# Kernel tuning notes

Hardware: AMD Instinct MI355X
Metric: run time of the kernel (lower is better)

Reference implementation:

```python
import jax, jax.numpy as jnp
import numpy as np
import math

D_MODEL = 1024
N_HEADS = 16
HEAD_DIM = D_MODEL // N_HEADS
PAD_INDEX = 0
NEG_INF = -1e9  # matches torch masked_fill value


def setup_inputs() -> dict:
    key = jax.random.key(0)
    ks = jax.random.split(key, 10)
    b, s = 2, 2048
    x = jax.random.normal(ks[0], (b, s, D_MODEL), dtype=jnp.float32)
    input_ids = jax.random.randint(ks[1], (b, s), 0, 32000, dtype=jnp.int64)
    scale = 1.0 / math.sqrt(D_MODEL)
    def lin(k):
        kw, kb = jax.random.split(k)
        W = jax.random.uniform(kw, (D_MODEL, D_MODEL), jnp.float32, -scale, scale)
        bb = jax.random.uniform(kb, (D_MODEL,), jnp.float32, -scale, scale)
        return W, bb
    Wq, bq = lin(ks[2])
    Wk, bk = lin(ks[3])
    Wv, bv = lin(ks[4])
    Wo, bo = lin(ks[5])
    return {"x": x, "input_ids": input_ids,
            "Wq": Wq, "bq": bq, "Wk": Wk, "bk": bk,
            "Wv": Wv, "bv": bv, "Wo": Wo, "bo": bo}


def reference(x, input_ids, Wq, bq, Wk, bk, Wv, bv, Wo, bo):
    b, s, _ = x.shape
    # torch nn.Linear: y = x @ W.T + b
    q = (x @ Wq.T + bq).reshape(b, s, N_HEADS, HEAD_DIM)
    k = (x @ Wk.T + bk).reshape(b, s, N_HEADS, HEAD_DIM)
    v = (x @ Wv.T + bv).reshape(b, s, N_HEADS, HEAD_DIM)
    # scores: [b, h, s, s]
    scores = jnp.einsum('bqhd,bkhd->bhqk', q, k) / math.sqrt(HEAD_DIM)
    pad_mask = (input_ids != PAD_INDEX)[:, None, None, :]          # [b,1,1,s] over keys
    causal = jnp.tril(jnp.ones((s, s), dtype=bool))[None, None]     # [1,1,s,s]
    final_mask = pad_mask & causal
    scores = jnp.where(final_mask, scores, NEG_INF)
    attn = jax.nn.softmax(scores, axis=-1)
    out = jnp.einsum('bhqk,bkhd->bqhd', attn, v).reshape(b, s, D_MODEL)
    return out @ Wo.T + bo
```

## Files before the change

### kernel.cpp

```cpp
#include <hip/hip_runtime.h>

#define DMODEL 1024
#define NHEADS 16
#define HDIM   64
#define BATCH  2
#define SEQ    2048
#define MROWS  (BATCH*SEQ)

typedef __bf16 bf16x8 __attribute__((ext_vector_type(8)));
typedef __bf16 bf16x4 __attribute__((ext_vector_type(4)));
typedef float floatx4 __attribute__((ext_vector_type(4)));

typedef const __attribute__((address_space(1))) void gvoid;
typedef __attribute__((address_space(3))) void lvoid;

template<int V>  struct ICi { static constexpr int  value = V; };
template<bool V> struct ICb { static constexpr bool value = V; };

__global__ void cast_all(const float* __restrict__ x,
                         const float* __restrict__ wq, const float* __restrict__ wk,
                         const float* __restrict__ wv, const float* __restrict__ wo,
                         __bf16* __restrict__ xb, __bf16* __restrict__ wqb,
                         __bf16* __restrict__ wkb, __bf16* __restrict__ wvb,
                         __bf16* __restrict__ wob)
{
  const int i = blockIdx.x * 256 + threadIdx.x;
  const float* s; __bf16* o; int off;
  if (i < MROWS*DMODEL/4) { s = x; o = xb; off = i; }
  else {
    const int r = i - MROWS*DMODEL/4;
    const int w = r >> 18;
    off = r & 262143;
    s = (w == 0) ? wq : (w == 1) ? wk : (w == 2) ? wv : wo;
    o = (w == 0) ? wqb : (w == 1) ? wkb : (w == 2) ? wvb : wob;
  }
  const float4 f = ((const float4*)s)[off];
  bf16x4 v = {(__bf16)f.x, (__bf16)f.y, (__bf16)f.z, (__bf16)f.w};
  *(bf16x4*)(o + off*4) = v;
}

template<int MODE>
__global__ __launch_bounds__(256, 3)
void gemm_nt(const unsigned short* __restrict__ A,
             const unsigned short* __restrict__ W0,
             const unsigned short* __restrict__ W1,
             const unsigned short* __restrict__ W2,
             const float* __restrict__ b0,
             const float* __restrict__ b1,
             const float* __restrict__ b2,
             unsigned short* __restrict__ qout,
             unsigned short* __restrict__ kout,
             unsigned short* __restrict__ vout,
             float* __restrict__ outf)
{
  const int K = DMODEL;
  __shared__ unsigned short As[2][128*32];
  __shared__ unsigned short Bs[2][128*32];
  const int tid  = threadIdx.x;
  const int wid  = tid >> 6;
  const int lane = tid & 63;

  const int lin = blockIdx.x;
  const int wg  = (MODE == 0) ? ((lin & 7)*96 + (lin >> 3))
                              : ((lin & 7)*32 + (lin >> 3));
  const int bx  = (MODE == 0) ? (wg % 24) : (wg & 7);
  const int by  = (MODE == 0) ? (wg / 24) : (wg >> 3);
  const int brow = by * 128;
  const int bcol = bx * 128;
  const int wr = (wid >> 1) * 64;
  const int wc = (wid & 1) * 64;

  int which = 0;
  const unsigned short* Bw = W0;
  const float* bias = b0;
  int bcolL = bcol;
  if (MODE == 0) {
    which = bcol >> 10;
    Bw   = which == 0 ? W0 : which == 1 ? W1 : W2;
    bias = which == 0 ? b0 : which == 1 ? b1 : b2;
    bcolL = bcol & 1023;
  }

  floatx4 acc[4][4] = {};

  const int sr = wid*16 + (lane >> 2);
  const int sc = (lane & 3) * 8;
  const int fr = lane & 15;
  const int fk = (lane >> 4) * 8;

#define GSTAGE(KT, B) do {                                                     \
    _Pragma("unroll")                                                          \
    for (int i_ = 0; i_ < 2; ++i_) {                                           \
      __builtin_amdgcn_global_load_lds(                                        \
          (gvoid*)(A + (size_t)(brow + i_*64 + sr)*K + (KT) + sc),             \
          (lvoid*)(As[B] + i_*2048 + wid*512), 16, 0, 0);                      \
      __builtin_amdgcn_global_load_lds(                                        \
          (gvoid*)(Bw + (size_t)(bcolL + i_*64 + sr)*K + (KT) + sc),           \
          (lvoid*)(Bs[B] + i_*2048 + wid*512), 16, 0, 0);                      \
    }                                                                          \
  } while (0)

  GSTAGE(0, 0);

  for (int kt = 0; kt < K; kt += 32) {
    const int cur = (kt >> 5) & 1;
    if (kt + 32 < K) {
      GSTAGE(kt + 32, cur ^ 1);
      asm volatile("s_waitcnt vmcnt(4)" ::: "memory");
    } else {
      asm volatile("s_waitcnt vmcnt(0)" ::: "memory");
    }
    __builtin_amdgcn_s_barrier();
    __builtin_amdgcn_sched_barrier(0);

    bf16x8 af[4], bfv[4];
#pragma unroll
    for (int m = 0; m < 4; ++m)
      af[m] = *(const bf16x8*)(As[cur] + (wr + m*16 + fr)*32 + fk);
#pragma unroll
    for (int n = 0; n < 4; ++n)
      bfv[n] = *(const bf16x8*)(Bs[cur] + (wc + n*16 + fr)*32 + fk);
    __builtin_amdgcn_s_setprio(1);
#pragma unroll
    for (int m = 0; m < 4; ++m)
#pragma unroll
      for (int n = 0; n < 4; ++n)
        acc[m][n] = __builtin_amdgcn_mfma_f32_16x16x32_bf16(af[m], bfv[n], acc[m][n], 0, 0, 0);
    __builtin_amdgcn_s_setprio(0);
    __builtin_amdgcn_s_barrier();
  }
#undef GSTAGE

  const int er = (lane >> 4) * 4;
  const int ec = lane & 15;
#pragma unroll
  for (int m = 0; m < 4; ++m) {
#pragma unroll
    for (int n = 0; n < 4; ++n) {
      const int colL = bcolL + wc + n*16 + ec;
      const float bv = bias[colL];
      const int rowb = brow + wr + m*16 + er;
      if (MODE == 0) {
        const int bi = rowb >> 11, s = rowb & 2047;
        const int hh = colL >> 6, dd = colL & 63;
        if (which == 2) {
          bf16x4 v4 = {(__bf16)(acc[m][n][0] + bv), (__bf16)(acc[m][n][1] + bv),
                       (__bf16)(acc[m][n][2] + bv), (__bf16)(acc[m][n][3] + bv)};
          *(bf16x4*)((__bf16*)vout + ((size_t)(bi*NHEADS + hh)*HDIM + dd)*SEQ + s) = v4;
        } else {
          __bf16* o = (__bf16*)((which == 0) ? qout : kout);
#pragma unroll
          for (int j = 0; j < 4; ++j)
            o[((size_t)(bi*NHEADS + hh)*SEQ + s + j)*HDIM + dd] = (__bf16)(acc[m][n][j] + bv);
        }
      } else {
#pragma unroll
        for (int j = 0; j < 4; ++j)
          outf[(size_t)(rowb + j)*DMODEL + colL] = acc[m][n][j] + bv;
      }
    }
  }
}

__global__ __launch_bounds__(256, 2)
void attn_fwd(const unsigned short* __restrict__ qb,
              const unsigned short* __restrict__ kb,
              const unsigned short* __restrict__ vtb,
              const int* __restrict__ ids,
              unsigned short* __restrict__ outb)
{
  const int hb = blockIdx.x;
  const int pr = blockIdx.y;
  const int h = hb & 15, bi = hb >> 4;

  const int tid = threadIdx.x, wid = tid >> 6, lane = tid & 63;
  const size_t hoff = (size_t)(bi*NHEADS + h) * SEQ * HDIM;
  const unsigned short* Qh  = qb  + hoff;
  const unsigned short* Kh  = kb  + hoff;
  const unsigned short* Vth = vtb + hoff;

  __shared__ unsigned short Ks[2][128*64];
  __shared__ unsigned short Vs[2][64*128];
  __shared__ unsigned short Ps[4][16*128];

  const int q_   = lane & 15;
  const int hi4  = lane >> 4;
  const int koff = hi4 * 4;
  const float SC2 = 0.125f * 1.44269504088896f;

  const int krow0 = tid >> 3;
  const int ksw   = ((tid & 7) ^ ((tid >> 3) & 7)) * 8;
  const int vrow0 = tid >> 4;
  const int vsw   = ((tid & 15) ^ ((tid >> 4) & 7)) * 8;
  unsigned short* Pw = Ps[wid];

#define STAGE(T, B) do {                                                       \
    const unsigned short* kbase_ = Kh + (size_t)(T)*128*HDIM;                  \
    const unsigned short* vbase_ = Vth + (size_t)(T)*128;                      \
    _Pragma("unroll")                                                          \
    for (int i_ = 0; i_ < 4; ++i_)                                             \
      __builtin_amdgcn_global_load_lds(                                        \
          (gvoid*)(kbase_ + (size_t)(krow0 + i_*32)*HDIM + ksw),               \
          (lvoid*)(Ks[B] + (tid + i_*256)*8), 16, 0, 0);                       \
    _Pragma("unroll")                                                          \
    for (int i_ = 0; i_ < 4; ++i_)                                             \
      __builtin_amdgcn_global_load_lds(                                        \
          (gvoid*)(vbase_ + (size_t)(vrow0 + i_*16)*SEQ + vsw),                \
          (lvoid*)(Vs[B] + (tid + i_*256)*8), 16, 0, 0);                       \
  } while (0)

  for (int half = 0; half < 2; ++half) {
    const int qt = half ? 31 - pr : pr;
    const int qbase = qt * 64;
    const int qg = qbase + wid*16 + q_;
    bf16x8 qf[2];
#pragma unroll
    for (int c = 0; c < 2; ++c)
      qf[c] = *(const bf16x8*)(Qh + (size_t)qg*HDIM + c*32 + hi4*8);

    float lsum = 0.f;
    floatx4 Oacc[4] = {};

    auto step = [&](auto TLc, auto Mc, int kb0, int bufc,
                    unsigned long long wma, unsigned long long wmb) {
      constexpr int TL = decltype(TLc)::value;
      constexpr bool MASKED = decltype(Mc)::value;

      floatx4 st[TL];
      __builtin_amdgcn_s_setprio(1);
#pragma unroll
      for (int t = 0; t < TL; ++t) {
        st[t] = (floatx4){0.f, 0.f, 0.f, 0.f};
        const int kr = t*16 + q_;
#pragma unroll
        for (int c = 0; c < 2; ++c) {
          const int cd = ((c*4 + hi4) ^ (kr & 7)) * 8;
          bf16x8 kf = *(const bf16x8*)(Ks[bufc] + kr*64 + cd);
          st[t] = __builtin_amdgcn_mfma_f32_16x16x32_bf16(kf, qf[c], st[t], 0, 0, 0);
        }
      }
      __builtin_amdgcn_s_setprio(0);

      float ps = 0.f;
#pragma unroll
      for (int t = 0; t < TL; ++t) {
        float p[4];
#pragma unroll
        for (int r = 0; r < 4; ++r) {
          float pv = exp2f(st[t][r] * SC2);
          if (MASKED) {
            const int ko = t*16 + koff + r;
            const unsigned long long wm = (t < 4) ? wma : wmb;
            const bool dead = ((kb0 + ko) > qg) || (((wm >> (ko & 63)) & 1ull) != 0ull);
            pv = dead ? 0.f : pv;
          }
          p[r] = pv;
          ps += pv;
        }
        bf16x4 pk = {(__bf16)p[0], (__bf16)p[1], (__bf16)p[2], (__bf16)p[3]};
        const int cl = t*2 + (hi4 >> 1);
        *(bf16x4*)(Pw + q_*128 + ((cl ^ (q_ & 7)) * 8) + ((hi4 & 1) * 4)) = pk;
      }
      lsum += ps;

      __builtin_amdgcn_s_setprio(1);
#pragma unroll
      for (int ks = 0; ks < TL/2; ++ks) {
        const int cl = ks*4 + hi4;
        bf16x8 pf = *(const bf16x8*)(Pw + q_*128 + ((cl ^ (q_ & 7)) * 8));
#pragma unroll
        for (int n = 0; n < 4; ++n) {
          const int d = n*16 + q_;
          bf16x8 vf = *(const bf16x8*)(Vs[bufc] + d*128 + ((cl ^ (d & 7)) * 8));
          Oacc[n] = __builtin_amdgcn_mfma_f32_16x16x32_bf16(pf, vf, Oacc[n], 0, 0, 0);
        }
      }
      __builtin_amdgcn_s_setprio(0);
    };

    const int nT = (qt >> 1) + 1;
    STAGE(0, 0);

    for (int kbv = 0; kbv < nT; ++kbv) {
      const int kb0 = kbv * 128;
      const int bufc = kbv & 1;
      const bool last = (kbv == nT - 1);
      const int pv0 = ids[bi*SEQ + kb0 + lane];
      const int pv1 = ids[bi*SEQ + kb0 + 64 + lane];
      if (!last) {
        STAGE(kbv + 1, bufc ^ 1);
        asm volatile("s_waitcnt vmcnt(8)" ::: "memory");
      } else {
        asm volatile("s_waitcnt vmcnt(0)" ::: "memory");
      }
      const unsigned long long wma = __ballot(pv0 == 0);
      const unsigned long long wmb = __ballot(pv1 == 0);
      __builtin_amdgcn_s_barrier();
      __builtin_amdgcn_sched_barrier(0);

      if (!last) {
        if ((wma | wmb) == 0ull) step(ICi<8>{}, ICb<false>{}, kb0, bufc, 0ull, 0ull);
        else                     step(ICi<8>{}, ICb<true >{}, kb0, bufc, wma, wmb);
      } else {
        if (qt & 1) step(ICi<8>{}, ICb<true>{}, kb0, bufc, wma, wmb);
        else        step(ICi<4>{}, ICb<true>{}, kb0, bufc, wma, wmb);
      }
      __builtin_amdgcn_s_barrier();
    }

    float lt = lsum + __shfl_xor(lsum, 16);
    lt += __shfl_xor(lt, 32);

#pragma unroll
    for (int r = 0; r < 4; ++r) {
      const float inv = 1.f / __shfl(lt, koff + r);
      const int row = bi*SEQ + qbase + wid*16 + koff + r;
#pragma unroll
      for (int n = 0; n < 4; ++n)
        ((__bf16*)outb)[(size_t)row*DMODEL + h*HDIM + n*16 + q_] = (__bf16)(Oacc[n][r] * inv);
    }
  }
#undef STAGE
}

extern "C" void kernel_launch(void* const* d_in, const int* in_sizes, int n_in,
                              void* d_out, int out_size, void* d_ws, size_t ws_size,
                              hipStream_t stream)
{
  const float* x  = (const float*)d_in[0];
  const int*   ids= (const int*)d_in[1];
  const float* Wq = (const float*)d_in[2];
  const float* bq = (const float*)d_in[3];
  const float* Wk = (const float*)d_in[4];
  const float* bk = (const float*)d_in[5];
  const float* Wv = (const float*)d_in[6];
  const float* bv = (const float*)d_in[7];
  const float* Wo = (const float*)d_in[8];
  const float* bo = (const float*)d_in[9];
  float* out = (float*)d_out;

  char* ws = (char*)d_ws;
  unsigned short* xb   = (unsigned short*)(ws);
  unsigned short* wqb  = (unsigned short*)(ws + ( 8u<<20));
  unsigned short* wkb  = (unsigned short*)(ws + (10u<<20));
  unsigned short* wvb  = (unsigned short*)(ws + (12u<<20));
  unsigned short* wob  = (unsigned short*)(ws + (14u<<20));
  unsigned short* qbuf = (unsigned short*)(ws + (16u<<20));
  unsigned short* kbuf = (unsigned short*)(ws + (24u<<20));
  unsigned short* vbuf = (unsigned short*)(ws + (32u<<20));
  unsigned short* abuf = (unsigned short*)(ws + (40u<<20));

  cast_all<<<8192, 256, 0, stream>>>(x, Wq, Wk, Wv, Wo,
                                     (__bf16*)xb, (__bf16*)wqb, (__bf16*)wkb,
                                     (__bf16*)wvb, (__bf16*)wob);

  gemm_nt<0><<<768, 256, 0, stream>>>(xb, wqb, wkb, wvb, bq, bk, bv,
                                      qbuf, kbuf, vbuf, nullptr);

  attn_fwd<<<dim3(32, 16), 256, 0, stream>>>(qbuf, kbuf, vbuf, ids, abuf);

  gemm_nt<1><<<256, 256, 0, stream>>>(abuf, wob, wob, wob, bo, bo, bo,
                                      nullptr, nullptr, nullptr, out);
}
```

Measured before the change: 113.4 us.

## Retile attention into 32-query, 32-key blocks and fold softmax scale into Q

Attention now launches 2048 blocks of 128 threads. Each block owns one 32-query tile and walks 32-key tiles, so the old pairing of two 64-query tiles per 256-thread block is gone. A snake ordering over tile indices is kept for causal load balance. The softmax scale and log2(e) factor are now applied in the Q projection epilogue, which removes a multiply per score. The aim is better occupancy and finer load balance, at the cost of more barriers and LDS staging per unit of work and more repeated K/V loads across blocks.

```diff
diff --git a/kernel.cpp b/kernel.cpp
--- a/kernel.cpp
+++ b/kernel.cpp
@@ -14,8 +14,9 @@
 typedef const __attribute__((address_space(1))) void gvoid;
 typedef __attribute__((address_space(3))) void lvoid;
 
-template<int V>  struct ICi { static constexpr int  value = V; };
 template<bool V> struct ICb { static constexpr bool value = V; };
+
+#define QSCALE 0.18033688011112042f
 
 __global__ void cast_all(const float* __restrict__ x,
                          const float* __restrict__ wq, const float* __restrict__ wk,
@@ -147,8 +148,14 @@
           bf16x4 v4 = {(__bf16)(acc[m][n][0] + bv), (__bf16)(acc[m][n][1] + bv),
                        (__bf16)(acc[m][n][2] + bv), (__bf16)(acc[m][n][3] + bv)};
           *(bf16x4*)((__bf16*)vout + ((size_t)(bi*NHEADS + hh)*HDIM + dd)*SEQ + s) = v4;
+        } else if (which == 0) {
+          __bf16* o = (__bf16*)qout;
+#pragma unroll
+          for (int j = 0; j < 4; ++j)
+            o[((size_t)(bi*NHEADS + hh)*SEQ + s + j)*HDIM + dd] =
+                (__bf16)((acc[m][n][j] + bv) * QSCALE);
         } else {
-          __bf16* o = (__bf16*)((which == 0) ? qout : kout);
+          __bf16* o = (__bf16*)kout;
 #pragma unroll
           for (int j = 0; j < 4; ++j)
             o[((size_t)(bi*NHEADS + hh)*SEQ + s + j)*HDIM + dd] = (__bf16)(acc[m][n][j] + bv);
@@ -162,15 +169,19 @@
   }
 }
 
-__global__ __launch_bounds__(256, 2)
+__global__ __launch_bounds__(128, 4)
 void attn_fwd(const unsigned short* __restrict__ qb,
               const unsigned short* __restrict__ kb,
               const unsigned short* __restrict__ vtb,
               const int* __restrict__ ids,
               unsigned short* __restrict__ outb)
 {
-  const int hb = blockIdx.x;
-  const int pr = blockIdx.y;
+  const int lin = blockIdx.x;
+  const int k8 = lin >> 8;
+  const int c8 = lin & 255;
+  const int hb = c8 & 31;
+  const int j  = c8 >> 5;
+  const int qt = k8*8 + ((k8 & 1) ? 7 - j : j);
   const int h = hb & 15, bi = hb >> 4;
 
   const int tid = threadIdx.x, wid = tid >> 6, lane = tid & 63;
@@ -179,148 +190,125 @@
   const unsigned short* Kh  = kb  + hoff;
   const unsigned short* Vth = vtb + hoff;
 
-  __shared__ unsigned short Ks[2][128*64];
-  __shared__ unsigned short Vs[2][64*128];
-  __shared__ unsigned short Ps[4][16*128];
+  __shared__ unsigned short Ks[2][32*64];
+  __shared__ unsigned short Vs[2][64*32];
+  __shared__ unsigned short Ps[2][16*32];
 
   const int q_   = lane & 15;
   const int hi4  = lane >> 4;
   const int koff = hi4 * 4;
-  const float SC2 = 0.125f * 1.44269504088896f;
-
-  const int krow0 = tid >> 3;
-  const int ksw   = ((tid & 7) ^ ((tid >> 3) & 7)) * 8;
-  const int vrow0 = tid >> 4;
-  const int vsw   = ((tid & 15) ^ ((tid >> 4) & 7)) * 8;
+  const int qg = qt*32 + wid*16 + q_;
+
+  bf16x8 qf[2];
+#pragma unroll
+  for (int c = 0; c < 2; ++c)
+    qf[c] = *(const bf16x8*)(Qh + (size_t)qg*HDIM + c*32 + hi4*8);
+
+  const int kr0 = tid >> 3;
+  const int kc  = ((tid & 7) ^ (kr0 & 7)) * 8;
+  const int vd0 = tid >> 2;
+  const int vc  = ((tid & 3) ^ (vd0 & 3)) * 8;
   unsigned short* Pw = Ps[wid];
 
 #define STAGE(T, B) do {                                                       \
-    const unsigned short* kbase_ = Kh + (size_t)(T)*128*HDIM;                  \
-    const unsigned short* vbase_ = Vth + (size_t)(T)*128;                      \
-    _Pragma("unroll")                                                          \
-    for (int i_ = 0; i_ < 4; ++i_)                                             \
-      __builtin_amdgcn_global_load_lds(                                        \
-          (gvoid*)(kbase_ + (size_t)(krow0 + i_*32)*HDIM + ksw),               \
-          (lvoid*)(Ks[B] + (tid + i_*256)*8), 16, 0, 0);                       \
-    _Pragma("unroll")                                                          \
-    for (int i_ = 0; i_ < 4; ++i_)                                             \
-      __builtin_amdgcn_global_load_lds(                                        \
-          (gvoid*)(vbase_ + (size_t)(vrow0 + i_*16)*SEQ + vsw),                \
-          (lvoid*)(Vs[B] + (tid + i_*256)*8), 16, 0, 0);                       \
+    const unsigned short* kb_ = Kh + (size_t)(T)*32*HDIM;                      \
+    const unsigned short* vb_ = Vth + (T)*32;                                  \
+    __builtin_amdgcn_global_load_lds((gvoid*)(kb_ + kr0*HDIM + kc),            \
+                                     (lvoid*)(Ks[B] + tid*8), 16, 0, 0);       \
+    __builtin_amdgcn_global_load_lds((gvoid*)(kb_ + (kr0+16)*HDIM + kc),       \
+                                     (lvoid*)(Ks[B] + (tid+128)*8), 16, 0, 0); \
+    __builtin_amdgcn_global_load_lds((gvoid*)(vb_ + (size_t)vd0*SEQ + vc),     \
+                                     (lvoid*)(Vs[B] + tid*8), 16, 0, 0);       \
+    __builtin_amdgcn_global_load_lds((gvoid*)(vb_ + (size_t)(vd0+32)*SEQ + vc),\
+                                     (lvoid*)(Vs[B] + (tid+128)*8), 16, 0, 0); \
   } while (0)
 
-  for (int half = 0; half < 2; ++half) {
-    const int qt = half ? 31 - pr : pr;
-    const int qbase = qt * 64;
-    const int qg = qbase + wid*16 + q_;
-    bf16x8 qf[2];
-#pragma unroll
-    for (int c = 0; c < 2; ++c)
-      qf[c] = *(const bf16x8*)(Qh + (size_t)qg*HDIM + c*32 + hi4*8);
-
-    float lsum = 0.f;
-    floatx4 Oacc[4] = {};
-
-    auto step = [&](auto TLc, auto Mc, int kb0, int bufc,
-                    unsigned long long wma, unsigned long long wmb) {
-      constexpr int TL = decltype(TLc)::value;
-      constexpr bool MASKED = decltype(Mc)::value;
-
-      floatx4 st[TL];
-      __builtin_amdgcn_s_setprio(1);
-#pragma unroll
-      for (int t = 0; t < TL; ++t) {
-        st[t] = (floatx4){0.f, 0.f, 0.f, 0.f};
-        const int kr = t*16 + q_;
-#pragma unroll
-        for (int c = 0; c < 2; ++c) {
-          const int cd = ((c*4 + hi4) ^ (kr & 7)) * 8;
-          bf16x8 kf = *(const bf16x8*)(Ks[bufc] + kr*64 + cd);
-          st[t] = __builtin_amdgcn_mfma_f32_16x16x32_bf16(kf, qf[c], st[t], 0, 0, 0);
+  float lsum = 0.f;
+  floatx4 Oacc[4] = {};
+
+  auto step = [&](auto Mc, int kb0, int bufc, unsigned int wm) {
+    constexpr bool MASKED = decltype(Mc)::value;
+
+    floatx4 st[2];
+    __builtin_amdgcn_s_setprio(1);
+#pragma unroll
+    for (int t = 0; t < 2; ++t) {
+      st[t] = (floatx4){0.f, 0.f, 0.f, 0.f};
+      const int kr = t*16 + q_;
+#pragma unroll
+      for (int c = 0; c < 2; ++c) {
+        bf16x8 kf = *(const bf16x8*)(Ks[bufc] + kr*64 + (((c*4 + hi4) ^ (q_ & 7)) * 8));
+        st[t] = __builtin_amdgcn_mfma_f32_16x16x32_bf16(kf, qf[c], st[t], 0, 0, 0);
+      }
+    }
+    __builtin_amdgcn_s_setprio(0);
+
+    float ps = 0.f;
+#pragma unroll
+    for (int t = 0; t < 2; ++t) {
+      float p[4];
+#pragma unroll
+      for (int r = 0; r < 4; ++r) {
+        float pv = exp2f(st[t][r]);
+        if (MASKED) {
+          const int ko = t*16 + koff + r;
+          const bool dead = ((kb0 + ko) > qg) || (((wm >> ko) & 1u) != 0u);
+          pv = dead ? 0.f : pv;
         }
+        p[r] = pv;
+        ps += pv;
       }
-      __builtin_amdgcn_s_setprio(0);
-
-      float ps = 0.f;
-#pragma unroll
-      for (int t = 0; t < TL; ++t) {
-        float p[4];
-#pragma unroll
-        for (int r = 0; r < 4; ++r) {
-          float pv = exp2f(st[t][r] * SC2);
-          if (MASKED) {
-            const int ko = t*16 + koff + r;
-            const unsigned long long wm = (t < 4) ? wma : wmb;
-            const bool dead = ((kb0 + ko) > qg) || (((wm >> (ko & 63)) & 1ull) != 0ull);
-            pv = dead ? 0.f : pv;
-          }
-          p[r] = pv;
-          ps += pv;
-        }
-        bf16x4 pk = {(__bf16)p[0], (__bf16)p[1], (__bf16)p[2], (__bf16)p[3]};
-        const int cl = t*2 + (hi4 >> 1);
-        *(bf16x4*)(Pw + q_*128 + ((cl ^ (q_ & 7)) * 8) + ((hi4 & 1) * 4)) = pk;
-      }
-      lsum += ps;
-
-      __builtin_amdgcn_s_setprio(1);
-#pragma unroll
-      for (int ks = 0; ks < TL/2; ++ks) {
-        const int cl = ks*4 + hi4;
-        bf16x8 pf = *(const bf16x8*)(Pw + q_*128 + ((cl ^ (q_ & 7)) * 8));
-#pragma unroll
-        for (int n = 0; n < 4; ++n) {
-          const int d = n*16 + q_;
-          bf16x8 vf = *(const bf16x8*)(Vs[bufc] + d*128 + ((cl ^ (d & 7)) * 8));
-          Oacc[n] = __builtin_amdgcn_mfma_f32_16x16x32_bf16(pf, vf, Oacc[n], 0, 0, 0);
-        }
-      }
-      __builtin_amdgcn_s_setprio(0);
-    };
-
-    const int nT = (qt >> 1) + 1;
-    STAGE(0, 0);
-
-    for (int kbv = 0; kbv < nT; ++kbv) {
-      const int kb0 = kbv * 128;
-      const int bufc = kbv & 1;
-      const bool last = (kbv == nT - 1);
-      const int pv0 = ids[bi*SEQ + kb0 + lane];
-      const int pv1 = ids[bi*SEQ + kb0 + 64 + lane];
-      if (!last) {
-        STAGE(kbv + 1, bufc ^ 1);
-        asm volatile("s_waitcnt vmcnt(8)" ::: "memory");
-      } else {
-        asm volatile("s_waitcnt vmcnt(0)" ::: "memory");
-      }
-      const unsigned long long wma = __ballot(pv0 == 0);
-      const unsigned long long wmb = __ballot(pv1 == 0);
-      __builtin_amdgcn_s_barrier();
-      __builtin_amdgcn_sched_barrier(0);
-
-      if (!last) {
-        if ((wma | wmb) == 0ull) step(ICi<8>{}, ICb<false>{}, kb0, bufc, 0ull, 0ull);
-        else                     step(ICi<8>{}, ICb<true >{}, kb0, bufc, wma, wmb);
-      } else {
-        if (qt & 1) step(ICi<8>{}, ICb<true>{}, kb0, bufc, wma, wmb);
-        else        step(ICi<4>{}, ICb<true>{}, kb0, bufc, wma, wmb);
-      }
-      __builtin_amdgcn_s_barrier();
-    }
-
-    float lt = lsum + __shfl_xor(lsum, 16);
-    lt += __shfl_xor(lt, 32);
-
-#pragma unroll
-    for (int r = 0; r < 4; ++r) {
-      const float inv = 1.f / __shfl(lt, koff + r);
-      const int row = bi*SEQ + qbase + wid*16 + koff + r;
-#pragma unroll
-      for (int n = 0; n < 4; ++n)
-        ((__bf16*)outb)[(size_t)row*DMODEL + h*HDIM + n*16 + q_] = (__bf16)(Oacc[n][r] * inv);
-    }
+      bf16x4 pk = {(__bf16)p[0], (__bf16)p[1], (__bf16)p[2], (__bf16)p[3]};
+      const int ch = t*2 + (hi4 >> 1);
+      *(bf16x4*)(Pw + q_*32 + ((ch ^ (q_ & 3)) * 8) + ((hi4 & 1) * 4)) = pk;
+    }
+    lsum += ps;
+
+    bf16x8 pf = *(const bf16x8*)(Pw + q_*32 + ((hi4 ^ (q_ & 3)) * 8));
+    __builtin_amdgcn_s_setprio(1);
+#pragma unroll
+    for (int n = 0; n < 4; ++n) {
+      const int d = n*16 + q_;
+      bf16x8 vf = *(const bf16x8*)(Vs[bufc] + d*32 + ((hi4 ^ (d & 3)) * 8));
+      Oacc[n] = __builtin_amdgcn_mfma_f32_16x16x32_bf16(pf, vf, Oacc[n], 0, 0, 0);
+    }
+    __builtin_amdgcn_s_setprio(0);
+  };
+
+  const int nT = qt + 1;
+  STAGE(0, 0);
+
+  for (int kbv = 0; kbv < nT; ++kbv) {
+    const int kb0 = kbv * 32;
+    const int bufc = kbv & 1;
+    const bool last = (kbv == nT - 1);
+    const int pv = ids[bi*SEQ + kb0 + (lane & 31)];
+    if (!last) {
+      STAGE(kbv + 1, bufc ^ 1);
+      asm volatile("s_waitcnt vmcnt(4)" ::: "memory");
+    } else {
+      asm volatile("s_waitcnt vmcnt(0)" ::: "memory");
+    }
+    const unsigned int wm = (unsigned int)__ballot(pv == 0);
+    __builtin_amdgcn_s_barrier();
+    __builtin_amdgcn_sched_barrier(0);
+
+    if (!last && wm == 0u) step(ICb<false>{}, kb0, bufc, 0u);
+    else                   step(ICb<true >{}, kb0, bufc, wm);
   }
 #undef STAGE
+
+  float lt = lsum + __shfl_xor(lsum, 16);
+  lt += __shfl_xor(lt, 32);
+
+#pragma unroll
+  for (int r = 0; r < 4; ++r) {
+    const float inv = 1.f / __shfl(lt, koff + r);
+    const int row = bi*SEQ + qt*32 + wid*16 + koff + r;
+#pragma unroll
+    for (int n = 0; n < 4; ++n)
+      ((__bf16*)outb)[(size_t)row*DMODEL + h*HDIM + n*16 + q_] = (__bf16)(Oacc[n][r] * inv);
+  }
 }
 
 extern "C" void kernel_launch(void* const* d_in, const int* in_sizes, int n_in,
@@ -357,7 +345,7 @@
   gemm_nt<0><<<768, 256, 0, stream>>>(xb, wqb, wkb, wvb, bq, bk, bv,
                                       qbuf, kbuf, vbuf, nullptr);
 
-  attn_fwd<<<dim3(32, 16), 256, 0, stream>>>(qbuf, kbuf, vbuf, ids, abuf);
+  attn_fwd<<<2048, 128, 0, stream>>>(qbuf, kbuf, vbuf, ids, abuf);
 
   gemm_nt<1><<<256, 256, 0, stream>>>(abuf, wob, wob, wob, bo, bo, bo,
                                       nullptr, nullptr, nullptr, out);
```

After: 127.9 us. 1.13x slower.
